# Performance work log

Measured on AMD Instinct MI355X. Metric: run time of the kernel, lower is better.

The kernel has to match this reference:

```python
import jax, jax.numpy as jnp
import numpy as np

H, W = 96, 96
THRESHOLD = 0.9
C = 256

def setup_inputs() -> dict:
    key = jax.random.key(0)
    k1, k2 = jax.random.split(key)
    return {
        "feature_query": jax.random.normal(k1, (C, H, W), jnp.float32),
        "feature_projection": jax.random.normal(k2, (C, H, W), jnp.float32),
    }

def reference(feature_query, feature_projection):
    c = feature_query.shape[0]
    # flatten spatial dims -> [C, N]; L2-normalize each pixel's descriptor over channels
    q = feature_query.reshape(c, -1)
    p = feature_projection.reshape(c, -1)
    q = q / jnp.linalg.norm(q, axis=0, keepdims=True)
    p = p / jnp.linalg.norm(p, axis=0, keepdims=True)
    # cosine similarity matrix [N, M] (GEMM)
    sim = jnp.einsum('cn,cm->nm', q, p)
    col_max = jnp.argmax(sim, axis=0)   # [M] best query row per projection column
    row_max = jnp.argmax(sim, axis=1)   # [N] best projection column per query row
    j = jnp.arange(sim.shape[1])
    q_idx = col_max                      # candidate query index for each column j
    sim_vals = sim[q_idx, j]
    # mutual nearest-neighbor + threshold (fixed-shape boolean mask instead of
    # a data-dependent python list, for jit compatibility)
    mutual = (row_max[q_idx] == j) & (sim_vals > THRESHOLD)
    # oneDim2TwoDim: (idx // W, idx % W), valid only if div+1 < H
    q_div, q_mod = q_idx // W, q_idx % W
    p_div, p_mod = j // W, j % W
    valid = mutual & (q_div + 1 < H) & (p_div + 1 < H)
    return sim, valid, q_idx, q_div, q_mod, p_div, p_mod
```

## Files before the change

kernel.cpp:

```cpp
#include <hip/hip_runtime.h>
#include <hip/hip_fp16.h>

#define N_PIX 9216
#define CCH 256
#define W_ 96
#define H_ 96
#define BM 128
#define BN 128
#define BK 16
#define TM 8
#define TN 8

typedef _Float16 half8_t __attribute__((ext_vector_type(8)));
typedef float f32x4_t __attribute__((ext_vector_type(4)));

__device__ __forceinline__ unsigned int mono_enc(float f) {
    unsigned int u = __float_as_uint(f);
    return (u & 0x80000000u) ? ~u : (u | 0x80000000u);
}
__device__ __forceinline__ float mono_dec(unsigned int e) {
    return __uint_as_float((e & 0x80000000u) ? (e ^ 0x80000000u) : ~e);
}

__device__ __forceinline__ void gload_lds16(const uint4* g, uint4* lds) {
    __builtin_amdgcn_global_load_lds(
        (const __attribute__((address_space(1))) unsigned int*)g,
        (__attribute__((address_space(3))) unsigned int*)lds, 16, 0, 0);
}


__global__ __launch_bounds__(256) void norms_kernel(const float* __restrict__ Q,
                                                    const float* __restrict__ P,
                                                    float* __restrict__ invq,
                                                    float* __restrict__ invp) {
    int n = blockIdx.x * blockDim.x + threadIdx.x;
    if (n >= N_PIX) return;
    float sq = 0.f, sp = 0.f;
    for (int c = 0; c < CCH; ++c) {
        float a = Q[(size_t)c * N_PIX + n];
        float b = P[(size_t)c * N_PIX + n];
        sq = fmaf(a, a, sq);
        sp = fmaf(b, b, sp);
    }
    invq[n] = 1.0f / sqrtf(sq);
    invp[n] = 1.0f / sqrtf(sp);
}

__device__ __forceinline__ int local_row(int ty, int i) {
    return (i < 4) ? (ty * 4 + i) : (64 + ty * 4 + (i - 4));
}
__device__ __forceinline__ int local_col(int tx, int j) {
    return (j < 4) ? (tx * 4 + j) : (64 + tx * 4 + (j - 4));
}

__global__ __launch_bounds__(256) void gemm_kernel(const float* __restrict__ Q,
                                                   const float* __restrict__ P,
                                                   const float* __restrict__ invq,
                                                   const float* __restrict__ invp,
                                                   float* __restrict__ sim,
                                                   unsigned long long* __restrict__ row_best,
                                                   unsigned long long* __restrict__ col_best) {
    __shared__ union SH {
        struct { float A[BK][BM]; float B[BK][BN]; } t;
        unsigned long long red[16][128];
    } sh;

    const int tid = threadIdx.x;
    const int tx = tid & 15;
    const int ty = tid >> 4;
    const int n0 = blockIdx.y * BM;
    const int m0 = blockIdx.x * BN;

    float acc[TM][TN];
#pragma unroll
    for (int i = 0; i < TM; ++i)
#pragma unroll
        for (int j = 0; j < TN; ++j) acc[i][j] = 0.f;

    for (int kk = 0; kk < CCH; kk += BK) {
#pragma unroll
        for (int rep = 0; rep < 2; ++rep) {
            int idx = tid + rep * 256;
            int row = idx >> 5;
            int c4  = idx & 31;
            float4 av = *(const float4*)&Q[(size_t)(kk + row) * N_PIX + n0 + c4 * 4];
            float4 bv = *(const float4*)&P[(size_t)(kk + row) * N_PIX + m0 + c4 * 4];
            *(float4*)&sh.t.A[row][c4 * 4] = av;
            *(float4*)&sh.t.B[row][c4 * 4] = bv;
        }
        __syncthreads();
#pragma unroll
        for (int k = 0; k < BK; ++k) {
            float a[TM], b[TN];
            *(float4*)&a[0] = *(const float4*)&sh.t.A[k][ty * 4];
            *(float4*)&a[4] = *(const float4*)&sh.t.A[k][ty * 4 + 64];
            *(float4*)&b[0] = *(const float4*)&sh.t.B[k][tx * 4];
            *(float4*)&b[4] = *(const float4*)&sh.t.B[k][tx * 4 + 64];
#pragma unroll
            for (int i = 0; i < TM; ++i)
#pragma unroll
                for (int j = 0; j < TN; ++j)
                    acc[i][j] = fmaf(a[i], b[j], acc[i][j]);
        }
        __syncthreads();
    }

    float iq[TM], ip[TN];
#pragma unroll
    for (int i = 0; i < TM; ++i) iq[i] = invq[n0 + local_row(ty, i)];
#pragma unroll
    for (int j = 0; j < TN; ++j) ip[j] = invp[m0 + local_col(tx, j)];
#pragma unroll
    for (int i = 0; i < TM; ++i)
#pragma unroll
        for (int j = 0; j < TN; ++j) acc[i][j] *= iq[i] * ip[j];

#pragma unroll
    for (int i = 0; i < TM; ++i) {
        int n = n0 + local_row(ty, i);
        float4 v0 = make_float4(acc[i][0], acc[i][1], acc[i][2], acc[i][3]);
        float4 v1 = make_float4(acc[i][4], acc[i][5], acc[i][6], acc[i][7]);
        float* dst = &sim[(size_t)n * N_PIX + m0];
        *(float4*)(dst + tx * 4) = v0;
        *(float4*)(dst + 64 + tx * 4) = v1;
    }

#pragma unroll
    for (int i = 0; i < TM; ++i) {
        float best = acc[i][0]; int bj = 0;
#pragma unroll
        for (int j = 1; j < TN; ++j)
            if (acc[i][j] > best) { best = acc[i][j]; bj = j; }
        unsigned int gcol = (unsigned int)(m0 + local_col(tx, bj));
        sh.red[tx][local_row(ty, i)] =
            ((unsigned long long)mono_enc(best) << 32) | (unsigned long long)(0xFFFFFFFFu - gcol);
    }
    __syncthreads();
    if (tid < 128) {
        unsigned long long best = sh.red[0][tid];
#pragma unroll
        for (int x = 1; x < 16; ++x) {
            unsigned long long v = sh.red[x][tid];
            if (v > best) best = v;
        }
        atomicMax(&row_best[n0 + tid], best);
    }
    __syncthreads();

#pragma unroll
    for (int j = 0; j < TN; ++j) {
        float best = acc[0][j]; int bi = 0;
#pragma unroll
        for (int i = 1; i < TM; ++i)
            if (acc[i][j] > best) { best = acc[i][j]; bi = i; }
        unsigned int grow = (unsigned int)(n0 + local_row(ty, bi));
        sh.red[ty][local_col(tx, j)] =
            ((unsigned long long)mono_enc(best) << 32) | (unsigned long long)(0xFFFFFFFFu - grow);
    }
    __syncthreads();
    if (tid < 128) {
        unsigned long long best = sh.red[0][tid];
#pragma unroll
        for (int x = 1; x < 16; ++x) {
            unsigned long long v = sh.red[x][tid];
            if (v > best) best = v;
        }
        atomicMax(&col_best[m0 + tid], best);
    }
}


__device__ __forceinline__ unsigned int pack_pair(float x, float y, float& rx, float& ry) {
    __half hx = __float2half(x), hy = __float2half(y);
    rx = x - __half2float(hx);
    ry = y - __half2float(hy);
    return (unsigned int)__half_as_ushort(hx) | ((unsigned int)__half_as_ushort(hy) << 16);
}

__global__ __launch_bounds__(256) void prep_kernel(const float* __restrict__ Q,
                                                   const float* __restrict__ P,
                                                   uint4* __restrict__ qh,
                                                   uint4* __restrict__ ql,
                                                   uint4* __restrict__ ph,
                                                   uint4* __restrict__ pl,
                                                   float* __restrict__ invq,
                                                   float* __restrict__ invp) {
    __shared__ float rq[4][64];
    __shared__ float rp[4][64];
    const int lane = threadIdx.x & 63;
    const int band = threadIdx.x >> 6;
    const int n = blockIdx.x * 64 + lane;
    float sq = 0.f, sp = 0.f;
    for (int kb = band * 8; kb < band * 8 + 8; ++kb) {
        float a[8], b[8];
#pragma unroll
        for (int t = 0; t < 8; ++t) {
            a[t] = Q[(size_t)(kb * 8 + t) * N_PIX + n];
            b[t] = P[(size_t)(kb * 8 + t) * N_PIX + n];
        }
#pragma unroll
        for (int t = 0; t < 8; ++t) {
            sq = fmaf(a[t], a[t], sq);
            sp = fmaf(b[t], b[t], sp);
        }
        uint4 vqh, vql, vph, vpl;
        unsigned int* uqh = (unsigned int*)&vqh;
        unsigned int* uql = (unsigned int*)&vql;
        unsigned int* uph = (unsigned int*)&vph;
        unsigned int* upl = (unsigned int*)&vpl;
#pragma unroll
        for (int j = 0; j < 4; ++j) {
            float r0, r1;
            uqh[j] = pack_pair(a[2 * j], a[2 * j + 1], r0, r1);
            uql[j] = (unsigned int)__half_as_ushort(__float2half(r0))
                   | ((unsigned int)__half_as_ushort(__float2half(r1)) << 16);
            uph[j] = pack_pair(b[2 * j], b[2 * j + 1], r0, r1);
            upl[j] = (unsigned int)__half_as_ushort(__float2half(r0))
                   | ((unsigned int)__half_as_ushort(__float2half(r1)) << 16);
        }
        size_t o = (size_t)kb * N_PIX + n;
        qh[o] = vqh; ql[o] = vql; ph[o] = vph; pl[o] = vpl;
    }
    rq[band][lane] = sq;
    rp[band][lane] = sp;
    __syncthreads();
    if (threadIdx.x < 64) {
        float tq = rq[0][lane] + rq[1][lane] + rq[2][lane] + rq[3][lane];
        float tp = rp[0][lane] + rp[1][lane] + rp[2][lane] + rp[3][lane];
        invq[n] = 1.0f / sqrtf(tq);
        invp[n] = 1.0f / sqrtf(tp);
    }
}

__global__ __launch_bounds__(512, 2) void mfma_gemm_kernel(
        const uint4* __restrict__ QH, const uint4* __restrict__ QL,
        const uint4* __restrict__ PH, const uint4* __restrict__ PL,
        const float* __restrict__ invq, const float* __restrict__ invp,
        float* __restrict__ sim,
        unsigned long long* __restrict__ row_best,
        unsigned long long* __restrict__ col_best) {
    const unsigned int bid = blockIdx.x;
    const unsigned int xcd = bid & 7u;
    const unsigned int nbl = bid >> 3;
    const unsigned int g   = nbl >> 3;
    const unsigned int ii  = nbl & 7u;
    const unsigned int by  = xcd * 6u + g % 6u;
    const unsigned int bx  = (g / 6u) * 8u + ii;

    const int tid = threadIdx.x;
    const int l  = tid & 63;
    const int w  = tid >> 6;
    const int rl = l & 15;
    const int kg = l >> 4;
    const int wr = w >> 1;
    const int wc = w & 1;
    const int n0 = (int)by * 192;
    const int m0 = (int)bx * 192;
    const int r0 = n0 + wr * 48;
    const int c0 = m0 + wc * 96;

    __shared__ union SH2 {
        uint4 stage[3][4][4][192];
        float st[8][16][108];
    } sh;

    const f32x4_t zero4 = {0.f, 0.f, 0.f, 0.f};
    f32x4_t acc[3][6];
#pragma unroll
    for (int i = 0; i < 3; ++i)
#pragma unroll
        for (int j = 0; j < 6; ++j) acc[i][j] = zero4;

    const int h3  = w >> 2;
    const int arr = w & 3;
    const uint4* gsrc = (arr == 0) ? (QH + n0) : (arr == 1) ? (QL + n0)
                      : (arr == 2) ? (PH + m0) : (PL + m0);

#define STAGE(step, buf)                                                        \
    {                                                                           \
        _Pragma("unroll")                                                       \
        for (int i = 0; i < 6; ++i) {                                           \
            const int rest = 2 * i + h3;                                        \
            const int kb = rest & 3;                                            \
            const int px0 = (rest >> 2) * 64;                                   \
            gload_lds16(gsrc + (size_t)((step) * 4 + kb) * N_PIX + px0 + l,     \
                        &sh.stage[buf][arr][kb][px0]);                          \
        }                                                                       \
    }

    STAGE(0, 0)
    STAGE(1, 1)
    asm volatile("s_waitcnt vmcnt(6)" ::: "memory");
    __builtin_amdgcn_s_barrier();
    __builtin_amdgcn_sched_barrier(0);

#pragma unroll
    for (int s = 0; s < 8; ++s) {
        const int cur = s % 3;
        if (s < 6) STAGE(s + 2, (s + 2) % 3)

        half8_t ah[3], al_[3], bh_[6], bl_[6];
#pragma unroll
        for (int f = 0; f < 3; ++f) {
            ah[f]  = *(const half8_t*)&sh.stage[cur][0][kg][wr * 48 + f * 16 + rl];
            al_[f] = *(const half8_t*)&sh.stage[cur][1][kg][wr * 48 + f * 16 + rl];
        }
#pragma unroll
        for (int f = 0; f < 6; ++f) {
            bh_[f] = *(const half8_t*)&sh.stage[cur][2][kg][wc * 96 + f * 16 + rl];
            bl_[f] = *(const half8_t*)&sh.stage[cur][3][kg][wc * 96 + f * 16 + rl];
        }
#pragma unroll
        for (int fr = 0; fr < 3; ++fr)
#pragma unroll
            for (int fc = 0; fc < 6; ++fc) {
                acc[fr][fc] = __builtin_amdgcn_mfma_f32_16x16x32_f16(ah[fr],  bh_[fc], acc[fr][fc], 0, 0, 0);
                acc[fr][fc] = __builtin_amdgcn_mfma_f32_16x16x32_f16(ah[fr],  bl_[fc], acc[fr][fc], 0, 0, 0);
                acc[fr][fc] = __builtin_amdgcn_mfma_f32_16x16x32_f16(al_[fr], bh_[fc], acc[fr][fc], 0, 0, 0);
            }

        if (s < 6) {
            asm volatile("s_waitcnt vmcnt(6)" ::: "memory");
        } else if (s == 6) {
            asm volatile("s_waitcnt vmcnt(0)" ::: "memory");
        }
        __builtin_amdgcn_s_barrier();
        __builtin_amdgcn_sched_barrier(0);
    }
#undef STAGE

    float iq[3][4];
#pragma unroll
    for (int fr = 0; fr < 3; ++fr) {
        const float4 v = *(const float4*)&invq[r0 + fr * 16 + kg * 4];
        iq[fr][0] = v.x; iq[fr][1] = v.y; iq[fr][2] = v.z; iq[fr][3] = v.w;
    }
    float ip[6];
#pragma unroll
    for (int fc = 0; fc < 6; ++fc) ip[fc] = invp[c0 + fc * 16 + rl];

#pragma unroll
    for (int fr = 0; fr < 3; ++fr)
#pragma unroll
        for (int fc = 0; fc < 6; ++fc)
#pragma unroll
            for (int j = 0; j < 4; ++j)
                acc[fr][fc][j] *= iq[fr][j] * ip[fc];

#pragma unroll
    for (int fr = 0; fr < 3; ++fr)
#pragma unroll
        for (int j = 0; j < 4; ++j) {
            float best = acc[fr][0][j];
            int bf = 0;
#pragma unroll
            for (int fc = 1; fc < 6; ++fc)
                if (acc[fr][fc][j] > best) { best = acc[fr][fc][j]; bf = fc; }
            const unsigned int gcol = (unsigned int)(c0 + bf * 16 + rl);
            unsigned long long key = ((unsigned long long)mono_enc(best) << 32)
                                   | (unsigned long long)(0xFFFFFFFFu - gcol);
#pragma unroll
            for (int m = 1; m < 16; m <<= 1) {
                unsigned long long o = __shfl_xor(key, m, 64);
                if (o > key) key = o;
            }
            if (rl == 0)
                atomicMax(&row_best[r0 + fr * 16 + kg * 4 + j], key);
        }

#pragma unroll
    for (int fc = 0; fc < 6; ++fc) {
        float best = acc[0][fc][0];
        unsigned int brow = (unsigned int)(r0 + kg * 4);
#pragma unroll
        for (int fr = 0; fr < 3; ++fr)
#pragma unroll
            for (int j = 0; j < 4; ++j) {
                float v = acc[fr][fc][j];
                unsigned int rr2 = (unsigned int)(r0 + fr * 16 + kg * 4 + j);
                if (v > best) { best = v; brow = rr2; }
            }
        unsigned long long key = ((unsigned long long)mono_enc(best) << 32)
                               | (unsigned long long)(0xFFFFFFFFu - brow);
#pragma unroll
        for (int m = 16; m < 64; m <<= 1) {
            unsigned long long o = __shfl_xor(key, m, 64);
            if (o > key) key = o;
        }
        if (kg == 0)
            atomicMax(&col_best[c0 + fc * 16 + rl], key);
    }

#pragma unroll
    for (int fr = 0; fr < 3; ++fr) {
        asm volatile("s_waitcnt lgkmcnt(0)" ::: "memory");
#pragma unroll
        for (int fc = 0; fc < 6; ++fc)
#pragma unroll
            for (int j = 0; j < 4; ++j)
                sh.st[w][kg * 4 + j][fc * 16 + rl] = acc[fr][fc][j];
        asm volatile("s_waitcnt lgkmcnt(0)" ::: "memory");
#pragma unroll
        for (int p = 0; p < 6; ++p) {
            const int flat = p * 64 + l;
            const int row = flat / 24;
            const int c4  = flat % 24;
            const f32x4_t v = *(const f32x4_t*)&sh.st[w][row][c4 * 4];
            const int gr = r0 + fr * 16 + row;
            __builtin_nontemporal_store(v, (f32x4_t*)(sim + (size_t)gr * N_PIX + c0 + c4 * 4));
        }
    }
}


__global__ __launch_bounds__(256) void epilogue_kernel(const unsigned long long* __restrict__ row_best,
                                                       const unsigned long long* __restrict__ col_best,
                                                       float* __restrict__ out) {
    int j = blockIdx.x * blockDim.x + threadIdx.x;
    if (j >= N_PIX) return;
    unsigned long long cb = col_best[j];
    unsigned int q_idx = 0xFFFFFFFFu - (unsigned int)(cb & 0xFFFFFFFFull);
    float simval = mono_dec((unsigned int)(cb >> 32));
    unsigned long long rb = row_best[q_idx];
    unsigned int rm = 0xFFFFFFFFu - (unsigned int)(rb & 0xFFFFFFFFull);
    bool mutual = (rm == (unsigned int)j) && (simval > 0.9f);
    int qd = (int)(q_idx / W_), qm = (int)(q_idx % W_);
    int pd = j / W_, pm = j % W_;
    bool valid = mutual && (qd + 1 < H_) && (pd + 1 < H_);
    size_t base = (size_t)N_PIX * N_PIX;
    out[base + 0 * (size_t)N_PIX + j] = valid ? 1.0f : 0.0f;
    out[base + 1 * (size_t)N_PIX + j] = (float)q_idx;
    out[base + 2 * (size_t)N_PIX + j] = (float)qd;
    out[base + 3 * (size_t)N_PIX + j] = (float)qm;
    out[base + 4 * (size_t)N_PIX + j] = (float)pd;
    out[base + 5 * (size_t)N_PIX + j] = (float)pm;
}

extern "C" void kernel_launch(void* const* d_in, const int* in_sizes, int n_in,
                              void* d_out, int out_size, void* d_ws, size_t ws_size,
                              hipStream_t stream) {
    const float* Q = (const float*)d_in[0];
    const float* P = (const float*)d_in[1];
    float* out = (float*)d_out;

    unsigned long long* row_best = (unsigned long long*)d_ws;
    unsigned long long* col_best = row_best + N_PIX;
    float* invq = (float*)(col_best + N_PIX);
    float* invp = invq + N_PIX;

    hipMemsetAsync(d_ws, 0, 2 * N_PIX * sizeof(unsigned long long), stream);

    const size_t base_bytes = 2 * N_PIX * sizeof(unsigned long long) + 2 * N_PIX * sizeof(float);
    const size_t arr_u4 = (size_t)(CCH / 8) * N_PIX;
    const size_t need = base_bytes + 4 * arr_u4 * sizeof(uint4);

    if (ws_size >= need) {
        uint4* qh = (uint4*)((char*)d_ws + base_bytes);
        uint4* ql = qh + arr_u4;
        uint4* ph = ql + arr_u4;
        uint4* pl = ph + arr_u4;

        prep_kernel<<<N_PIX / 64, 256, 0, stream>>>(Q, P, qh, ql, ph, pl, invq, invp);
        mfma_gemm_kernel<<<2304, 512, 0, stream>>>(qh, ql, ph, pl, invq, invp,
                                                   out, row_best, col_best);
    } else {
        norms_kernel<<<N_PIX / 256, 256, 0, stream>>>(Q, P, invq, invp);
        dim3 grid(N_PIX / BN, N_PIX / BM);
        gemm_kernel<<<grid, 256, 0, stream>>>(Q, P, invq, invp, out, row_best, col_best);
    }

    epilogue_kernel<<<N_PIX / 256, 256, 0, stream>>>(row_best, col_best, out);
}
```

Measured before the change: 485.8 us.

## Double-buffer GEMM staging in chunks, fold memset into prep, widen prep grid

New measurement: 465.7 us. 4.1% less time.

```diff
diff --git a/kernel.cpp b/kernel.cpp
--- a/kernel.cpp
+++ b/kernel.cpp
@@ -184,24 +184,31 @@
                                                    uint4* __restrict__ ph,
                                                    uint4* __restrict__ pl,
                                                    float* __restrict__ invq,
-                                                   float* __restrict__ invp) {
-    __shared__ float rq[4][64];
-    __shared__ float rp[4][64];
-    const int lane = threadIdx.x & 63;
-    const int band = threadIdx.x >> 6;
-    const int n = blockIdx.x * 64 + lane;
+                                                   float* __restrict__ invp,
+                                                   unsigned long long* __restrict__ best01) {
+    __shared__ float rq[16][17];
+    __shared__ float rp[16][17];
+    const int t = threadIdx.x;
+    const int n16 = t & 15;
+    const int ks = t >> 4;
+    const int n = blockIdx.x * 16 + n16;
+
+    if (t < 32) best01[blockIdx.x * 32 + t] = 0ULL;
+
     float sq = 0.f, sp = 0.f;
-    for (int kb = band * 8; kb < band * 8 + 8; ++kb) {
+#pragma unroll
+    for (int kk = 0; kk < 2; ++kk) {
+        const int kb = ks * 2 + kk;
         float a[8], b[8];
 #pragma unroll
-        for (int t = 0; t < 8; ++t) {
-            a[t] = Q[(size_t)(kb * 8 + t) * N_PIX + n];
-            b[t] = P[(size_t)(kb * 8 + t) * N_PIX + n];
-        }
-#pragma unroll
-        for (int t = 0; t < 8; ++t) {
-            sq = fmaf(a[t], a[t], sq);
-            sp = fmaf(b[t], b[t], sp);
+        for (int u = 0; u < 8; ++u) {
+            a[u] = Q[(size_t)(kb * 8 + u) * N_PIX + n];
+            b[u] = P[(size_t)(kb * 8 + u) * N_PIX + n];
+        }
+#pragma unroll
+        for (int u = 0; u < 8; ++u) {
+            sq = fmaf(a[u], a[u], sq);
+            sp = fmaf(b[u], b[u], sp);
         }
         uint4 vqh, vql, vph, vpl;
         unsigned int* uqh = (unsigned int*)&vqh;
@@ -221,14 +228,20 @@
         size_t o = (size_t)kb * N_PIX + n;
         qh[o] = vqh; ql[o] = vql; ph[o] = vph; pl[o] = vpl;
     }
-    rq[band][lane] = sq;
-    rp[band][lane] = sp;
+    rq[ks][n16] = sq;
+    rp[ks][n16] = sp;
     __syncthreads();
-    if (threadIdx.x < 64) {
-        float tq = rq[0][lane] + rq[1][lane] + rq[2][lane] + rq[3][lane];
-        float tp = rp[0][lane] + rp[1][lane] + rp[2][lane] + rp[3][lane];
-        invq[n] = 1.0f / sqrtf(tq);
-        invp[n] = 1.0f / sqrtf(tp);
+    if (t < 16) {
+        float s = 0.f;
+#pragma unroll
+        for (int x = 0; x < 16; ++x) s += rq[x][t];
+        invq[blockIdx.x * 16 + t] = 1.0f / sqrtf(s);
+    } else if (t < 32) {
+        const int tt = t - 16;
+        float s = 0.f;
+#pragma unroll
+        for (int x = 0; x < 16; ++x) s += rp[x][tt];
+        invp[blockIdx.x * 16 + tt] = 1.0f / sqrtf(s);
     }
 }
 
@@ -260,74 +273,104 @@
     const int c0 = m0 + wc * 96;
 
     __shared__ union SH2 {
-        uint4 stage[3][4][4][192];
-        float st[8][16][108];
+        uint4 stage[2][3072];
+        float st[8][16][100];
     } sh;
 
-    const f32x4_t zero4 = {0.f, 0.f, 0.f, 0.f};
     f32x4_t acc[3][6];
 #pragma unroll
     for (int i = 0; i < 3; ++i)
 #pragma unroll
-        for (int j = 0; j < 6; ++j) acc[i][j] = zero4;
-
-    const int h3  = w >> 2;
-    const int arr = w & 3;
-    const uint4* gsrc = (arr == 0) ? (QH + n0) : (arr == 1) ? (QL + n0)
-                      : (arr == 2) ? (PH + m0) : (PL + m0);
-
-#define STAGE(step, buf)                                                        \
-    {                                                                           \
-        _Pragma("unroll")                                                       \
-        for (int i = 0; i < 6; ++i) {                                           \
-            const int rest = 2 * i + h3;                                        \
-            const int kb = rest & 3;                                            \
-            const int px0 = (rest >> 2) * 64;                                   \
-            gload_lds16(gsrc + (size_t)((step) * 4 + kb) * N_PIX + px0 + l,     \
-                        &sh.stage[buf][arr][kb][px0]);                          \
-        }                                                                       \
-    }
-
-    STAGE(0, 0)
-    STAGE(1, 1)
-    asm volatile("s_waitcnt vmcnt(6)" ::: "memory");
-    __builtin_amdgcn_s_barrier();
+        for (int j = 0; j < 6; ++j) acc[i][j] = {0.f, 0.f, 0.f, 0.f};
+
+    const uint4* srcc[6];
+#pragma unroll
+    for (int c = 0; c < 6; ++c) {
+        const int f = c * 512 + tid;
+        const int r = f / 768;
+        const int gg2 = f - r * 768;
+        const int kb = gg2 / 192;
+        const int px = gg2 - kb * 192;
+        const uint4* base = (r == 0) ? (QH + n0) : (r == 1) ? (PH + m0)
+                          : (r == 2) ? (PL + m0) : (QL + n0);
+        srcc[c] = base + (size_t)kb * N_PIX + px;
+    }
+
+#define ISSUE2(cA, cB, wb)                                                     \
+    gload_lds16(srcc[cA], &sh.stage[wb][(cA) * 512 + w * 64]);                 \
+    gload_lds16(srcc[cB], &sh.stage[wb][(cB) * 512 + w * 64]);
+
+#define ENTRY(N)                                                               \
+    asm volatile("s_waitcnt vmcnt(" #N ")" ::: "memory");                      \
+    __builtin_amdgcn_s_barrier();                                              \
     __builtin_amdgcn_sched_barrier(0);
 
 #pragma unroll
-    for (int s = 0; s < 8; ++s) {
-        const int cur = s % 3;
-        if (s < 6) STAGE(s + 2, (s + 2) % 3)
-
-        half8_t ah[3], al_[3], bh_[6], bl_[6];
-#pragma unroll
-        for (int f = 0; f < 3; ++f) {
-            ah[f]  = *(const half8_t*)&sh.stage[cur][0][kg][wr * 48 + f * 16 + rl];
-            al_[f] = *(const half8_t*)&sh.stage[cur][1][kg][wr * 48 + f * 16 + rl];
-        }
-#pragma unroll
-        for (int f = 0; f < 6; ++f) {
-            bh_[f] = *(const half8_t*)&sh.stage[cur][2][kg][wc * 96 + f * 16 + rl];
-            bl_[f] = *(const half8_t*)&sh.stage[cur][3][kg][wc * 96 + f * 16 + rl];
-        }
+    for (int c = 0; c < 6; ++c)
+        gload_lds16(srcc[c], &sh.stage[0][c * 512 + w * 64]);
+#pragma unroll
+    for (int c = 0; c < 6; ++c) srcc[c] += (size_t)4 * N_PIX;
+
+    const int aoff = kg * 192 + wr * 48 + rl;
+    const int boff = kg * 192 + wc * 96 + rl;
+
+#pragma unroll
+    for (int t = 0; t < 8; ++t) {
+        const int rb = t & 1, wb = (t + 1) & 1;
+        const uint4* Bb = &sh.stage[rb][0];
+        half8_t ahi[3], bhi[6];
+
+        ENTRY(3)
+        if (t < 7) { ISSUE2(0, 1, wb) }
+#pragma unroll
+        for (int fr = 0; fr < 3; ++fr) ahi[fr] = *(const half8_t*)&Bb[aoff + fr * 16];
+#pragma unroll
+        for (int fc = 0; fc < 6; ++fc) bhi[fc] = *(const half8_t*)&Bb[768 + boff + fc * 16];
+        __builtin_amdgcn_s_setprio(1);
 #pragma unroll
         for (int fr = 0; fr < 3; ++fr)
 #pragma unroll
-            for (int fc = 0; fc < 6; ++fc) {
-                acc[fr][fc] = __builtin_amdgcn_mfma_f32_16x16x32_f16(ah[fr],  bh_[fc], acc[fr][fc], 0, 0, 0);
-                acc[fr][fc] = __builtin_amdgcn_mfma_f32_16x16x32_f16(ah[fr],  bl_[fc], acc[fr][fc], 0, 0, 0);
-                acc[fr][fc] = __builtin_amdgcn_mfma_f32_16x16x32_f16(al_[fr], bh_[fc], acc[fr][fc], 0, 0, 0);
-            }
-
-        if (s < 6) {
-            asm volatile("s_waitcnt vmcnt(6)" ::: "memory");
-        } else if (s == 6) {
-            asm volatile("s_waitcnt vmcnt(0)" ::: "memory");
-        }
-        __builtin_amdgcn_s_barrier();
-        __builtin_amdgcn_sched_barrier(0);
-    }
-#undef STAGE
+            for (int fc = 0; fc < 6; ++fc)
+                acc[fr][fc] = __builtin_amdgcn_mfma_f32_16x16x32_f16(ahi[fr], bhi[fc], acc[fr][fc], 0, 0, 0);
+        __builtin_amdgcn_s_setprio(0);
+
+        if (t < 7) { ENTRY(3) } else { ENTRY(1) }
+        if (t < 7) { ISSUE2(2, 3, wb) }
+        {
+            half8_t blo[6];
+#pragma unroll
+            for (int fc = 0; fc < 6; ++fc) blo[fc] = *(const half8_t*)&Bb[1536 + boff + fc * 16];
+            __builtin_amdgcn_s_setprio(1);
+#pragma unroll
+            for (int fr = 0; fr < 3; ++fr)
+#pragma unroll
+                for (int fc = 0; fc < 6; ++fc)
+                    acc[fr][fc] = __builtin_amdgcn_mfma_f32_16x16x32_f16(ahi[fr], blo[fc], acc[fr][fc], 0, 0, 0);
+            __builtin_amdgcn_s_setprio(0);
+        }
+
+        if (t < 7) { ENTRY(4) } else { ENTRY(0) }
+        if (t < 7) { ISSUE2(4, 5, wb) }
+        {
+            half8_t alo[3];
+#pragma unroll
+            for (int fr = 0; fr < 3; ++fr) alo[fr] = *(const half8_t*)&Bb[2304 + aoff + fr * 16];
+            __builtin_amdgcn_s_setprio(1);
+#pragma unroll
+            for (int fr = 0; fr < 3; ++fr)
+#pragma unroll
+                for (int fc = 0; fc < 6; ++fc)
+                    acc[fr][fc] = __builtin_amdgcn_mfma_f32_16x16x32_f16(alo[fr], bhi[fc], acc[fr][fc], 0, 0, 0);
+            __builtin_amdgcn_s_setprio(0);
+        }
+
+        if (t < 7) {
+#pragma unroll
+            for (int c = 0; c < 6; ++c) srcc[c] += (size_t)4 * N_PIX;
+        }
+    }
+#undef ISSUE2
+#undef ENTRY
 
     float iq[3][4];
 #pragma unroll
@@ -448,8 +491,6 @@
     float* invq = (float*)(col_best + N_PIX);
     float* invp = invq + N_PIX;
 
-    hipMemsetAsync(d_ws, 0, 2 * N_PIX * sizeof(unsigned long long), stream);
-
     const size_t base_bytes = 2 * N_PIX * sizeof(unsigned long long) + 2 * N_PIX * sizeof(float);
     const size_t arr_u4 = (size_t)(CCH / 8) * N_PIX;
     const size_t need = base_bytes + 4 * arr_u4 * sizeof(uint4);
@@ -460,10 +501,12 @@
         uint4* ph = ql + arr_u4;
         uint4* pl = ph + arr_u4;
 
-        prep_kernel<<<N_PIX / 64, 256, 0, stream>>>(Q, P, qh, ql, ph, pl, invq, invp);
+        prep_kernel<<<N_PIX / 16, 256, 0, stream>>>(Q, P, qh, ql, ph, pl, invq, invp,
+                                                    (unsigned long long*)d_ws);
         mfma_gemm_kernel<<<2304, 512, 0, stream>>>(qh, ql, ph, pl, invq, invp,
                                                    out, row_best, col_best);
     } else {
+        hipMemsetAsync(d_ws, 0, 2 * N_PIX * sizeof(unsigned long long), stream);
         norms_kernel<<<N_PIX / 256, 256, 0, stream>>>(Q, P, invq, invp);
         dim3 grid(N_PIX / BN, N_PIX / BM);
         gemm_kernel<<<grid, 256, 0, stream>>>(Q, P, invq, invp, out, row_best, col_best);
```
